# Optimization experiments

Measured on AMD Instinct MI355X. Metric: run time of the kernel, lower is better.

## Reference

```python
import jax, jax.numpy as jnp
import numpy as np

# ---- config (matches init_kwargs) ----
B, IN_CH, H, W_SP = 8, 1, 256, 256
WIDTH, M1, M2, NL, OUT_CH = 64, 12, 12, 4, 1
FC_HID = 128


def _gelu(a):
    # torch nn.GELU default = exact erf form
    return jax.nn.gelu(a, approximate=False)


def _spectral_conv2d(x, w1, w2):
    """x: [B, Cin, H, W]; w1/w2: [Cin, Cout, M1, M2, 2] -> [B, Cout, H, W]."""
    Bn, Cin, Hn, Wn = x.shape
    Cout = w1.shape[1]
    x_ft = jnp.fft.rfft2(x, axes=(-2, -1))          # [B, Cin, H, W//2+1] complex
    w1c = w1[..., 0] + 1j * w1[..., 1]
    w2c = w2[..., 0] + 1j * w2[..., 1]
    top = jnp.einsum('bixy,ioxy->boxy', x_ft[:, :, :M1, :M2], w1c)
    bot = jnp.einsum('bixy,ioxy->boxy', x_ft[:, :, -M1:, :M2], w2c)
    out_ft = jnp.zeros((Bn, Cout, Hn, Wn // 2 + 1), dtype=x_ft.dtype)
    out_ft = out_ft.at[:, :, :M1, :M2].set(top)
    out_ft = out_ft.at[:, :, -M1:, :M2].set(bot)
    return jnp.fft.irfft2(out_ft, s=(Hn, Wn), axes=(-2, -1))


def setup_inputs() -> dict:
    key = jax.random.key(0)
    ks = jax.random.split(key, 8)
    scale = 1.0 / (WIDTH * WIDTH)
    inp = {
        'x': jax.random.normal(ks[0], (B, IN_CH, H, W_SP)),
        'fc0_w': jax.random.normal(ks[1], (WIDTH, IN_CH + 2)) * 0.3,
        'fc0_b': jnp.zeros((WIDTH,)),
        # spectral weights stacked over layers: [NL, Cin, Cout, M1, M2, 2]
        'w1': scale * jax.random.uniform(ks[2], (NL, WIDTH, WIDTH, M1, M2, 2)),
        'w2': scale * jax.random.uniform(ks[3], (NL, WIDTH, WIDTH, M1, M2, 2)),
        # 1x1 conv weights: [NL, Cout, Cin] and bias [NL, Cout]
        'pw_w': jax.random.normal(ks[4], (NL, WIDTH, WIDTH)) * (1.0 / np.sqrt(WIDTH)),
        'pw_b': jnp.zeros((NL, WIDTH)),
        'fc1_w': jax.random.normal(ks[5], (FC_HID, WIDTH)) * (1.0 / np.sqrt(WIDTH)),
        'fc1_b': jnp.zeros((FC_HID,)),
        'fc2_w': jax.random.normal(ks[6], (OUT_CH, FC_HID)) * (1.0 / np.sqrt(FC_HID)),
        'fc2_b': jnp.zeros((OUT_CH,)),
    }
    return {k: v.astype(jnp.float32) for k, v in inp.items()}


def reference(x, fc0_w, fc0_b, w1, w2, pw_w, pw_b, fc1_w, fc1_b, fc2_w, fc2_b):
    Bn, _, Hn, Wn = x.shape
    # positional grid in [0, 1], concatenated on channel dim
    gx = jnp.broadcast_to(jnp.linspace(0.0, 1.0, Hn)[None, None, :, None], (Bn, 1, Hn, Wn))
    gy = jnp.broadcast_to(jnp.linspace(0.0, 1.0, Wn)[None, None, None, :], (Bn, 1, Hn, Wn))
    h = jnp.concatenate([x, gx.astype(x.dtype), gy.astype(x.dtype)], axis=1)  # [B, in+2, H, W]
    # lift (fc0): Linear over channels (torch weight layout [out, in])
    h = jnp.einsum('bcxy,wc->bwxy', h, fc0_w) + fc0_b[None, :, None, None]
    for i in range(NL):
        x1 = _spectral_conv2d(h, w1[i], w2[i])
        x2 = jnp.einsum('bixy,oi->boxy', h, pw_w[i]) + pw_b[i][None, :, None, None]
        h = x1 + x2
        if i < NL - 1:
            h = _gelu(h)
    # projection head
    h = jnp.einsum('bwxy,fw->bfxy', h, fc1_w) + fc1_b[None, :, None, None]
    h = _gelu(h)
    h = jnp.einsum('bfxy,of->boxy', h, fc2_w) + fc2_b[None, :, None, None]
    return h  # [B, out_channels, H, W]
```

## Files before the change

### kernel.cpp

```cpp
#include <hip/hip_runtime.h>
#include <hip/hip_bf16.h>

#define FC0_F   0
#define FC0B_F  192
#define PWB_F   16640
#define FC1B_F  25088
#define FC2_F   25216
#define FC2B_F  25344
#define PHW_F   25408
#define PHH_F   31552
#define FLAG_F  44032
#define PWA_HI_U 512
#define PWA_LO_U 16896
#define FC1A_HI_U 33792
#define FC1A_LO_U 41984
#define TWI_HI_U 88192
#define TWI_LO_U 96384
#define TWF_HI_U 104576
#define TWF_LO_U 112768
#define HB_OFF_U  131072
#define GG_OFF_U  33685504
#define FO_OFF_F  18415616
#define WS_NEED   74842112
#define NT11 60161

typedef short bf16x8 __attribute__((ext_vector_type(8)));
typedef float f32x4  __attribute__((ext_vector_type(4)));

union FU10 { float f; unsigned u; };
__device__ __forceinline__ float bfu2f(unsigned short u) { FU10 v; v.u = ((unsigned)u) << 16; return v.f; }
__device__ __forceinline__ unsigned short f2bfu(float f) {
  FU10 v; v.f = f; unsigned b = v.u;
  return (unsigned short)((b + 0x7FFFu + ((b >> 16) & 1u)) >> 16);
}
__device__ __forceinline__ unsigned pk2bf(float a, float b) {
  return (unsigned)f2bfu(a) | ((unsigned)f2bfu(b) << 16);
}
__device__ __forceinline__ float gelu10(float v) {
  float s = v * 0.7071067811865475f;
  float a = fabsf(s);
  float t = __builtin_amdgcn_rcpf(1.0f + 0.3275911f * a);
  float p = t*(0.254829592f + t*(-0.284496736f + t*(1.421413741f
          + t*(-1.453152027f + t*1.061405429f))));
  float er = 1.0f - p * __expf(-a * a);
  er = copysignf(er, s);
  return 0.5f * v * (1.0f + er);
}
__device__ __forceinline__ float rdw10(const __hip_bfloat16* h, const float* f,
                                       long i, int isf32) {
  return isf32 ? f[i] : __bfloat162float(h[i]);
}

__global__ __launch_bounds__(256) void kf10_fill(__hip_bfloat16* outH, float code) {
  outH[(size_t)blockIdx.x * 256 + threadIdx.x] = __float2bfloat16(code);
}

__global__ __launch_bounds__(64) void kd10_detect(const unsigned short* Xh, float* Wf) {
  if (threadIdx.x == 0 && blockIdx.x == 0) {
    int ok = 1;
    for (int k = 0; k < 128; ++k) {
      unsigned short u = Xh[2 * k];
      unsigned e = (u >> 7) & 0xFF;
      if (!(u == 0 || (e >= 0x60 && e <= 0x88))) ok = 0;
    }
    Wf[FLAG_F] = ok ? 0.0f : 1.0f;
  }
}

__global__ __launch_bounds__(256) void kt10_tables(
    const __hip_bfloat16* f0h, const float* f0f,
    const __hip_bfloat16* f0bh, const float* f0bf,
    const __hip_bfloat16* pwh, const float* pwf,
    const __hip_bfloat16* pwbh, const float* pwbf,
    const __hip_bfloat16* f1h, const float* f1f,
    const __hip_bfloat16* f1bh, const float* f1bf,
    const __hip_bfloat16* f2h, const float* f2f,
    const __hip_bfloat16* f2bh, const float* f2bf,
    float* Wf) {
  unsigned short* Wu = (unsigned short*)Wf;
  const int isf32 = (Wf[FLAG_F] != 0.0f);
  const int stride = gridDim.x * blockDim.x;
  for (int n0 = blockIdx.x * blockDim.x + threadIdx.x; n0 < NT11; n0 += stride) {
    int n = n0;
    if (n < 192) { Wf[FC0_F + n] = rdw10(f0h, f0f, n, isf32); continue; }
    n -= 192;
    if (n < 64)  { Wf[FC0B_F + n] = rdw10(f0bh, f0bf, n, isf32); continue; }
    n -= 64;
    if (n < 256) { Wf[PWB_F + n] = rdw10(pwbh, pwbf, n, isf32); continue; }
    n -= 256;
    if (n < 8192) {
      float v = rdw10(f1h, f1f, n, isf32);
      unsigned short hi = f2bfu(v);
      Wu[FC1A_HI_U + n] = hi;
      Wu[FC1A_LO_U + n] = f2bfu(v - bfu2f(hi));
      continue;
    }
    n -= 8192;
    if (n < 128) { Wf[FC1B_F + n] = rdw10(f1bh, f1bf, n, isf32); continue; }
    n -= 128;
    if (n < 128) { Wf[FC2_F + n] = rdw10(f2h, f2f, n, isf32); continue; }
    n -= 128;
    if (n < 1)   { Wf[FC2B_F + n] = rdw10(f2bh, f2bf, 0, isf32); continue; }
    n -= 1;
    if (n < 6144) { int w = n / 24, r = n % 24, ky = r >> 1, part = r & 1;
      int idx = (w * ky) & 255; float a = idx * (1.0f/128.0f);
      Wf[PHW_F + n] = part ? sinpif(a) : cospif(a); continue; }
    n -= 6144;
    if (n < 12288) { int xx = n / 48, r = n % 48, kx = r >> 1, part = r & 1;
      int kxa = (kx < 12) ? kx : kx + 232;
      int idx = (xx * kxa) & 255; float a = idx * (1.0f/128.0f);
      Wf[PHH_F + n] = part ? sinpif(a) : cospif(a); continue; }
    n -= 12288;
    if (n < 16384) {
      float v = rdw10(pwh, pwf, n, isf32);
      unsigned short hi = f2bfu(v);
      Wu[PWA_HI_U + n] = hi;
      Wu[PWA_LO_U + n] = f2bfu(v - bfu2f(hi));
      continue;
    }
    n -= 16384;
    if (n < 8192) {
      int w = n >> 5, k = n & 31;
      float v;
      if (k == 0)      v = 1.0f / 65536.0f;
      else if (k < 12) { int idx = (w*k) & 255;
        v =  2.0f * cospif(idx * (1.0f/128.0f)) * (1.0f/65536.0f); }
      else if (k < 23) { int ky = k - 11; int idx = (w*ky) & 255;
        v = -2.0f * sinpif(idx * (1.0f/128.0f)) * (1.0f/65536.0f); }
      else v = 0.0f;
      unsigned short hi = f2bfu(v);
      Wu[TWI_HI_U + n] = hi;
      Wu[TWI_LO_U + n] = f2bfu(v - bfu2f(hi));
      continue;
    }
    n -= 8192;
    {
      int r = n >> 8, w = n & 255;
      float v;
      if (r < 12)      { int idx = (w*r) & 255;  v =  cospif(idx * (1.0f/128.0f)); }
      else if (r < 24) { int ky = r - 12; int idx = (w*ky) & 255;
                         v = -sinpif(idx * (1.0f/128.0f)); }
      else v = 0.0f;
      unsigned short hi = f2bfu(v);
      Wu[TWF_HI_U + n] = hi;
      Wu[TWF_LO_U + n] = f2bfu(v - bfu2f(hi));
    }
  }
}

__global__ __launch_bounds__(256) void kl11_lift(const __hip_bfloat16* Xh, const float* Xf,
                                                 const float* Wf,
                                                 __hip_bfloat16* HB, __hip_bfloat16* GG) {
  __shared__ __align__(16) char smem[32768];
  unsigned short* gbT = (unsigned short*)smem;
  const unsigned short* Wu = (const unsigned short*)Wf;
  const int rid = ((blockIdx.x & 7) << 8) | (blockIdx.x >> 3);
  const int b = rid >> 8, x = rid & 255;
  const int t = threadIdx.x;
  const int w = t;
  const int l15 = t & 15, g = (t >> 4) & 3, wv = t >> 6;
  const int isf32 = (Wf[FLAG_F] != 0.0f);
  float xv = isf32 ? Xf[(size_t)(b*256 + x)*256 + w]
                   : __bfloat162float(Xh[(size_t)(b*256 + x)*256 + w]);
  float gx = x * (1.0f/255.0f), gy = w * (1.0f/255.0f);
  unsigned hbreg[32];
#pragma unroll
  for (int cp = 0; cp < 32; ++cp) {
    int c = cp*2;
    float h0 = xv*Wf[FC0_F + c*3]     + gx*Wf[FC0_F + c*3 + 1]
             + gy*Wf[FC0_F + c*3 + 2] + Wf[FC0B_F + c];
    float h1 = xv*Wf[FC0_F + c*3 + 3] + gx*Wf[FC0_F + c*3 + 4]
             + gy*Wf[FC0_F + c*3 + 5] + Wf[FC0B_F + c + 1];
    unsigned pk = pk2bf(h0, h1);
    hbreg[cp] = pk;
    *(unsigned short*)(smem + (((c+0)*512 + w*2) ^ (((c+0) & 7) << 4))) =
        (unsigned short)(pk & 0xFFFFu);
    *(unsigned short*)(smem + (((c+1)*512 + w*2) ^ (((c+1) & 7) << 4))) =
        (unsigned short)(pk >> 16);
  }
  {
    uint4* hbW = (uint4*)(HB + (size_t)(b*256 + x)*16384) + w*8;
#pragma unroll
    for (int j = 0; j < 8; ++j)
      hbW[j] = make_uint4(hbreg[j*4], hbreg[j*4+1], hbreg[j*4+2], hbreg[j*4+3]);
  }
  __syncthreads();

  f32x4 g0 = {0.f, 0.f, 0.f, 0.f}, g1 = {0.f, 0.f, 0.f, 0.f};
  const int crow = wv*16 + l15;
  const int rswz = (crow & 7) << 4;
#pragma unroll
  for (int kk = 0; kk < 8; ++kk) {
    const int k0 = kk*32;
    bf16x8 af  = *(const bf16x8*)(smem + ((crow*512 + (k0 + g*8)*2) ^ rswz));
    bf16x8 b0h = *(const bf16x8*)(Wu + TWF_HI_U + l15*256 + k0 + g*8);
    bf16x8 b0l = *(const bf16x8*)(Wu + TWF_LO_U + l15*256 + k0 + g*8);
    bf16x8 b1h = *(const bf16x8*)(Wu + TWF_HI_U + (16 + l15)*256 + k0 + g*8);
    bf16x8 b1l = *(const bf16x8*)(Wu + TWF_LO_U + (16 + l15)*256 + k0 + g*8);
    g0 = __builtin_amdgcn_mfma_f32_16x16x32_bf16(af, b0h, g0, 0, 0, 0);
    g0 = __builtin_amdgcn_mfma_f32_16x16x32_bf16(af, b0l, g0, 0, 0, 0);
    g1 = __builtin_amdgcn_mfma_f32_16x16x32_bf16(af, b1h, g1, 0, 0, 0);
    g1 = __builtin_amdgcn_mfma_f32_16x16x32_bf16(af, b1l, g1, 0, 0, 0);
  }
  __syncthreads();
#pragma unroll
  for (int ntk = 0; ntk < 2; ++ntk) {
    int kyt = ntk*16 + l15;
    if (kyt < 24) {
      f32x4 gg = ntk ? g1 : g0;
#pragma unroll
      for (int rr = 0; rr < 4; ++rr)
        gbT[(wv*16 + g*4 + rr)*24 + kyt] = f2bfu(gg[rr]);
    }
  }
  __syncthreads();
  unsigned* GGrow = (unsigned*)((unsigned short*)GG + (size_t)(b*256 + x)*1536);
  const unsigned* st32 = (const unsigned*)gbT;
#pragma unroll
  for (int j = 0; j < 3; ++j) GGrow[j*256 + t] = st32[j*256 + t];
}

__global__ __launch_bounds__(256) void ks10_spec(const float* Wf, const __hip_bfloat16* GG,
    const __hip_bfloat16* w1h, const float* w1f,
    const __hip_bfloat16* w2h, const float* w2f,
    float* Fo, int l) {
  __shared__ float pbufA[6400];
  __shared__ float Fbuf[1536];
  const int blk = (blockIdx.x & 7) * 24 + (blockIdx.x >> 3);
  const int b = blk / 24, kx = blk % 24;
  const int t = threadIdx.x;
  const int isf32 = (Wf[FLAG_F] != 0.0f);
  {
    const int i = t & 63, q = t >> 6;
    float fr[12], fi[12];
#pragma unroll
    for (int k = 0; k < 12; ++k) { fr[k] = 0.0f; fi[k] = 0.0f; }
    for (int j = 0; j < 64; ++j) {
      int x = q*64 + j;
      const uint4* gp = (const uint4*)((const unsigned short*)GG
                        + (size_t)(b*256 + x)*1536 + i*24);
      uint4 u0 = gp[0], u1 = gp[1], u2 = gp[2];
      float cc = Wf[PHH_F + x*48 + 2*kx], ss = Wf[PHH_F + x*48 + 2*kx + 1];
      unsigned uu[12] = {u0.x, u0.y, u0.z, u0.w, u1.x, u1.y, u1.z, u1.w,
                         u2.x, u2.y, u2.z, u2.w};
#pragma unroll
      for (int k = 0; k < 12; ++k) {
        unsigned ure = uu[k >> 1], uim = uu[6 + (k >> 1)];
        float gr = bfu2f((unsigned short)((k & 1) ? (ure >> 16) : (ure & 0xFFFFu)));
        float gi = bfu2f((unsigned short)((k & 1) ? (uim >> 16) : (uim & 0xFFFFu)));
        fr[k] += gr*cc + gi*ss;
        fi[k] += gi*cc - gr*ss;
      }
    }
#pragma unroll
    for (int k = 0; k < 12; ++k) {
      pbufA[q*1600 + i*25 + 2*k]     = fr[k];
      pbufA[q*1600 + i*25 + 2*k + 1] = fi[k];
    }
  }
  __syncthreads();
#pragma unroll
  for (int j = 0; j < 6; ++j) {
    int idx = j*256 + t;
    int cc = idx / 24, m = idx - cc*24;
    Fbuf[idx] = pbufA[cc*25 + m] + pbufA[1600 + cc*25 + m]
              + pbufA[3200 + cc*25 + m] + pbufA[4800 + cc*25 + m];
  }
  __syncthreads();
  {
    const int o = t & 63, q = t >> 6;
    float br[12], bi[12];
#pragma unroll
    for (int k = 0; k < 12; ++k) { br[k] = 0.0f; bi[k] = 0.0f; }
    const int kxe = (kx < 12) ? kx : kx - 12;
    const __hip_bfloat16* wh = (kx < 12) ? w1h : w2h;
    const float*         wfp = (kx < 12) ? w1f : w2f;
    for (int i = q*16; i < q*16 + 16; ++i) {
      size_t widx = ((size_t)((l*64 + i)*64 + o))*288 + (size_t)kxe*24;
      float wr_[12], wi_[12];
      if (isf32) {
        const float* wp = wfp + widx;
#pragma unroll
        for (int k = 0; k < 12; ++k) { wr_[k] = wp[2*k]; wi_[k] = wp[2*k + 1]; }
      } else {
        const uint4* wp = (const uint4*)((const unsigned short*)wh + widx);
        uint4 u0 = wp[0], u1 = wp[1], u2 = wp[2];
        unsigned uu[12] = {u0.x, u0.y, u0.z, u0.w, u1.x, u1.y, u1.z, u1.w,
                           u2.x, u2.y, u2.z, u2.w};
#pragma unroll
        for (int k = 0; k < 12; ++k) {
          wr_[k] = bfu2f((unsigned short)(uu[k] & 0xFFFFu));
          wi_[k] = bfu2f((unsigned short)(uu[k] >> 16));
        }
      }
      const float* Fp = Fbuf + i*24;
#pragma unroll
      for (int k = 0; k < 12; ++k) {
        float Fr = Fp[k], Fi = Fp[12 + k];
        br[k] += Fr*wr_[k] - Fi*wi_[k];
        bi[k] += Fr*wi_[k] + Fi*wr_[k];
      }
    }
#pragma unroll
    for (int k = 0; k < 12; ++k) {
      pbufA[q*1536 + k*128 + o*2]     = br[k];
      pbufA[q*1536 + k*128 + o*2 + 1] = bi[k];
    }
  }
  __syncthreads();
#pragma unroll
  for (int j = 0; j < 6; ++j) {
    int n = j*256 + t;
    int ky = n >> 7, r = n & 127;
    Fo[((size_t)(b*12 + ky)*24 + kx)*128 + r] =
        pbufA[n] + pbufA[1536 + n] + pbufA[3072 + n] + pbufA[4608 + n];
  }
}

__global__ __launch_bounds__(256) void ky13_layer(const float* __restrict__ Wf,
                                                  __hip_bfloat16* __restrict__ HB,
                                                  __hip_bfloat16* __restrict__ GG,
                                                  const float* __restrict__ Fo,
                                                  __hip_bfloat16* __restrict__ outH,
                                                  float* __restrict__ outF,
                                                  int l, int last) {
  __shared__ __align__(16) char smem[32768];
  unsigned short* gbT   = (unsigned short*)smem;
  unsigned*       gbT32 = (unsigned*)smem;
  const unsigned short* Wu = (const unsigned short*)Wf;
  const int rid = ((blockIdx.x & 7) << 8) | (blockIdx.x >> 3);
  const int b = rid >> 8, x = rid & 255;
  const int t = threadIdx.x;
  const int l15 = t & 15, g = (t >> 4) & 3, wv = t >> 6;

  unsigned short* HBu = (unsigned short*)(HB + (size_t)(b*256 + x)*16384);
  unsigned short* GGu = (unsigned short*)GG + (size_t)(b*256 + x)*1536;

  const int w0w = wv*64;
  bf16x8 bh[4][2];
#pragma unroll
  for (int nt = 0; nt < 4; ++nt) {
    int wpx = w0w + nt*16 + l15;
#pragma unroll
    for (int kt = 0; kt < 2; ++kt)
      bh[nt][kt] = *(const bf16x8*)(HBu + (size_t)wpx*64 + kt*32 + g*8);
  }

  { int o = t >> 2, cu = t & 3; gbT32[o*16 + 12 + cu] = 0u; }
  {
    const float* phx = Wf + PHH_F + x*48;
#pragma unroll 1
    for (int j = 0; j < 3; ++j) {
      int p = j*256 + t; int ky = p >> 6, o = p & 63;
      const float2* Fop = (const float2*)(Fo + (size_t)(b*12 + ky)*3072) + o;
      float gr = 0.0f, gi = 0.0f;
#pragma unroll
      for (int kx = 0; kx < 24; ++kx) {
        float2 f = Fop[kx*64];
        float cc = phx[2*kx], ss = phx[2*kx + 1];
        gr += f.x*cc - f.y*ss;
        gi += f.x*ss + f.y*cc;
      }
      gbT[o*32 + ky] = f2bfu(gr);
      gbT[o*32 + (ky ? (11 + ky) : 23)] = f2bfu(gi);
    }
  }

  bf16x8 bi[4][2];
#pragma unroll
  for (int nt = 0; nt < 4; ++nt) {
    int wpx = w0w + nt*16 + l15;
    bi[nt][0] = *(const bf16x8*)(Wu + TWI_HI_U + wpx*32 + g*8);
    bi[nt][1] = *(const bf16x8*)(Wu + TWI_LO_U + wpx*32 + g*8);
  }
  bf16x8 apw[4][2][2];
#pragma unroll
  for (int mt = 0; mt < 4; ++mt)
#pragma unroll
    for (int kt = 0; kt < 2; ++kt) {
      int off = l*4096 + (mt*16 + l15)*64 + kt*32 + g*8;
      apw[mt][kt][0] = *(const bf16x8*)(Wu + PWA_HI_U + off);
      apw[mt][kt][1] = *(const bf16x8*)(Wu + PWA_LO_U + off);
    }
  float bias[4][4];
#pragma unroll
  for (int mt = 0; mt < 4; ++mt)
#pragma unroll
    for (int r = 0; r < 4; ++r)
      bias[mt][r] = Wf[PWB_F + l*64 + mt*16 + g*4 + r];

  __syncthreads();
  bf16x8 ainv[4];
#pragma unroll
  for (int mt = 0; mt < 4; ++mt)
    ainv[mt] = *(const bf16x8*)(gbT + (mt*16 + l15)*32 + g*8);
  __syncthreads();

#pragma unroll
  for (int nt = 0; nt < 4; ++nt) {
    const int wpx = w0w + nt*16 + l15;
#pragma unroll
    for (int mt = 0; mt < 4; ++mt) {
      f32x4 acc = {bias[mt][0], bias[mt][1], bias[mt][2], bias[mt][3]};
      acc = __builtin_amdgcn_mfma_f32_16x16x32_bf16(ainv[mt],      bi[nt][0], acc, 0, 0, 0);
      acc = __builtin_amdgcn_mfma_f32_16x16x32_bf16(ainv[mt],      bi[nt][1], acc, 0, 0, 0);
      acc = __builtin_amdgcn_mfma_f32_16x16x32_bf16(apw[mt][0][0], bh[nt][0], acc, 0, 0, 0);
      acc = __builtin_amdgcn_mfma_f32_16x16x32_bf16(apw[mt][0][1], bh[nt][0], acc, 0, 0, 0);
      acc = __builtin_amdgcn_mfma_f32_16x16x32_bf16(apw[mt][1][0], bh[nt][1], acc, 0, 0, 0);
      acc = __builtin_amdgcn_mfma_f32_16x16x32_bf16(apw[mt][1][1], bh[nt][1], acc, 0, 0, 0);
      float v0 = acc[0], v1 = acc[1], v2 = acc[2], v3 = acc[3];
      if (!last) { v0 = gelu10(v0); v1 = gelu10(v1); v2 = gelu10(v2); v3 = gelu10(v3); }
      const int c0 = mt*16 + g*4;
      uint2 pk; pk.x = pk2bf(v0, v1); pk.y = pk2bf(v2, v3);
      if (!last) {
        *(uint2*)(HBu + (size_t)wpx*64 + c0) = pk;
        *(unsigned short*)(smem + (((c0+0)*512 + wpx*2) ^ (((c0+0) & 7) << 4))) = f2bfu(v0);
        *(unsigned short*)(smem + (((c0+1)*512 + wpx*2) ^ (((c0+1) & 7) << 4))) = f2bfu(v1);
        *(unsigned short*)(smem + (((c0+2)*512 + wpx*2) ^ (((c0+2) & 7) << 4))) = f2bfu(v2);
        *(unsigned short*)(smem + (((c0+3)*512 + wpx*2) ^ (((c0+3) & 7) << 4))) = f2bfu(v3);
      } else {
        *(uint2*)(smem + ((wpx*128 + c0*2) ^ ((wpx & 7) << 4))) = pk;
      }
    }
  }

  if (!last) {
    __syncthreads();
    f32x4 g0 = {0.f, 0.f, 0.f, 0.f}, g1 = {0.f, 0.f, 0.f, 0.f};
    const int crow = wv*16 + l15;
    const int rswz = (crow & 7) << 4;
#pragma unroll
    for (int kk = 0; kk < 8; ++kk) {
      const int k0 = kk*32;
      bf16x8 af  = *(const bf16x8*)(smem + ((crow*512 + (k0 + g*8)*2) ^ rswz));
      bf16x8 b0h = *(const bf16x8*)(Wu + TWF_HI_U + l15*256 + k0 + g*8);
      bf16x8 b0l = *(const bf16x8*)(Wu + TWF_LO_U + l15*256 + k0 + g*8);
      bf16x8 b1h = *(const bf16x8*)(Wu + TWF_HI_U + (16 + l15)*256 + k0 + g*8);
      bf16x8 b1l = *(const bf16x8*)(Wu + TWF_LO_U + (16 + l15)*256 + k0 + g*8);
      g0 = __builtin_amdgcn_mfma_f32_16x16x32_bf16(af, b0h, g0, 0, 0, 0);
      g0 = __builtin_amdgcn_mfma_f32_16x16x32_bf16(af, b0l, g0, 0, 0, 0);
      g1 = __builtin_amdgcn_mfma_f32_16x16x32_bf16(af, b1h, g1, 0, 0, 0);
      g1 = __builtin_amdgcn_mfma_f32_16x16x32_bf16(af, b1l, g1, 0, 0, 0);
    }
    __syncthreads();
#pragma unroll
    for (int ntk = 0; ntk < 2; ++ntk) {
      int kyt = ntk*16 + l15;
      if (kyt < 24) {
        f32x4 gg = ntk ? g1 : g0;
#pragma unroll
        for (int rr = 0; rr < 4; ++rr)
          gbT[(wv*16 + g*4 + rr)*24 + kyt] = f2bfu(gg[rr]);
      }
    }
    __syncthreads();
    unsigned* GGrow = (unsigned*)GGu;
    const unsigned* st32 = (const unsigned*)gbT;
#pragma unroll
    for (int j = 0; j < 3; ++j) GGrow[j*256 + t] = st32[j*256 + t];
  } else {
    __syncthreads();
    const int isf32 = (Wf[FLAG_F] != 0.0f);
    bf16x8 bh2[4][2];
#pragma unroll
    for (int nt = 0; nt < 4; ++nt) {
      int wpx = w0w + nt*16 + l15;
#pragma unroll
      for (int kt = 0; kt < 2; ++kt)
        bh2[nt][kt] = *(const bf16x8*)(smem +
            ((wpx*128 + kt*64 + g*16) ^ ((wpx & 7) << 4)));
    }
    float s[4] = {0.0f, 0.0f, 0.0f, 0.0f};
#pragma unroll 2
    for (int mt = 0; mt < 8; ++mt) {
      const int arow = (mt*16 + l15)*64 + g*8;
      bf16x8 a0h = *(const bf16x8*)(Wu + FC1A_HI_U + arow);
      bf16x8 a0l = *(const bf16x8*)(Wu + FC1A_LO_U + arow);
      bf16x8 a1h = *(const bf16x8*)(Wu + FC1A_HI_U + arow + 32);
      bf16x8 a1l = *(const bf16x8*)(Wu + FC1A_LO_U + arow + 32);
      float f1b[4], f2v[4];
#pragma unroll
      for (int r = 0; r < 4; ++r) {
        f1b[r] = Wf[FC1B_F + mt*16 + g*4 + r];
        f2v[r] = Wf[FC2_F  + mt*16 + g*4 + r];
      }
#pragma unroll
      for (int nt = 0; nt < 4; ++nt) {
        f32x4 acc = {f1b[0], f1b[1], f1b[2], f1b[3]};
        acc = __builtin_amdgcn_mfma_f32_16x16x32_bf16(a0h, bh2[nt][0], acc, 0, 0, 0);
        acc = __builtin_amdgcn_mfma_f32_16x16x32_bf16(a0l, bh2[nt][0], acc, 0, 0, 0);
        acc = __builtin_amdgcn_mfma_f32_16x16x32_bf16(a1h, bh2[nt][1], acc, 0, 0, 0);
        acc = __builtin_amdgcn_mfma_f32_16x16x32_bf16(a1l, bh2[nt][1], acc, 0, 0, 0);
#pragma unroll
        for (int r = 0; r < 4; ++r)
          s[nt] += gelu10(acc[r]) * f2v[r];
      }
    }
    const float fc2b = Wf[FC2B_F];
#pragma unroll
    for (int nt = 0; nt < 4; ++nt) {
      float v = s[nt];
      v += __shfl_xor(v, 16);
      v += __shfl_xor(v, 32);
      if (g == 0) {
        size_t idx = (size_t)(b*256 + x)*256 + (w0w + nt*16 + l15);
        if (isf32) outF[idx] = v + fc2b;
        else       outH[idx] = __float2bfloat16(v + fc2b);
      }
    }
  }
}

extern "C" void kernel_launch(void* const* d_in, const int* in_sizes, int n_in,
                              void* d_out, int out_size, void* d_ws, size_t ws_size,
                              hipStream_t stream) {
  (void)out_size;
  __hip_bfloat16* outH = (__hip_bfloat16*)d_out;
  float*          outF = (float*)d_out;
  float*          Wf   = (float*)d_ws;
  __hip_bfloat16* HB   = (__hip_bfloat16*)d_ws + HB_OFF_U;
  __hip_bfloat16* GG   = (__hip_bfloat16*)d_ws + GG_OFF_U;
  float*          Fo   = (float*)d_ws + FO_OFF_F;

  static const int EXP_SZ[11] = {524288, 192, 64, 4718592, 4718592,
                                 16384, 256, 8192, 128, 128, 1};
  if (n_in != 11) { kf10_fill<<<2048, 256, 0, stream>>>(outH, 27648.0f); return; }
  for (int i = 0; i < 11; ++i) {
    if (in_sizes[i] != EXP_SZ[i]) {
      kf10_fill<<<2048, 256, 0, stream>>>(outH, 28672.0f + 256.0f * (float)i);
      return;
    }
  }
  if (ws_size < (size_t)WS_NEED) {
    int q = (int)(ws_size >> 25); if (q > 31) q = 31;
    kf10_fill<<<2048, 256, 0, stream>>>(outH, 4096.0f + 32.0f * (float)q);
    return;
  }

  kd10_detect<<<1, 64, 0, stream>>>((const unsigned short*)d_in[0], Wf);
  kt10_tables<<<64, 256, 0, stream>>>(
      (const __hip_bfloat16*)d_in[1], (const float*)d_in[1],
      (const __hip_bfloat16*)d_in[2], (const float*)d_in[2],
      (const __hip_bfloat16*)d_in[5], (const float*)d_in[5],
      (const __hip_bfloat16*)d_in[6], (const float*)d_in[6],
      (const __hip_bfloat16*)d_in[7], (const float*)d_in[7],
      (const __hip_bfloat16*)d_in[8], (const float*)d_in[8],
      (const __hip_bfloat16*)d_in[9], (const float*)d_in[9],
      (const __hip_bfloat16*)d_in[10], (const float*)d_in[10],
      Wf);
  kl11_lift<<<2048, 256, 0, stream>>>((const __hip_bfloat16*)d_in[0],
                                      (const float*)d_in[0], Wf, HB, GG);
  for (int l = 0; l < 4; ++l) {
    ks10_spec<<<192, 256, 0, stream>>>(Wf, GG,
        (const __hip_bfloat16*)d_in[3], (const float*)d_in[3],
        (const __hip_bfloat16*)d_in[4], (const float*)d_in[4],
        Fo, l);
    ky13_layer<<<2048, 256, 0, stream>>>(Wf, HB, GG, Fo, outH, outF,
                                         l, (l == 3) ? 1 : 0);
  }
}
```

Before: 691.2 us.

## Widen spectral kernel to 1024 threads and swizzle layer-kernel LDS tile

The spectral-mixing kernel now launches 1024 threads per block instead of 256. Each wave handles a quarter of the previous x-range and input-channel range, and partial sums are combined in shared memory over four serialized accumulate rounds with barriers. This targets low occupancy, since only 192 blocks run on a large GPU. Separately, the layer kernel's 64x32 bf16 shared tile uses an XOR swizzle on byte addresses to reduce LDS bank conflicts on the transposed writes and MFMA operand reads. The extra barriers and serialized shared-memory reductions add overhead in exchange.

```diff
diff --git a/kernel.cpp b/kernel.cpp
--- a/kernel.cpp
+++ b/kernel.cpp
@@ -49,6 +49,9 @@
 __device__ __forceinline__ float rdw10(const __hip_bfloat16* h, const float* f,
                                        long i, int isf32) {
   return isf32 ? f[i] : __bfloat162float(h[i]);
+}
+__device__ __forceinline__ int gsw17(int o, int br) {
+  return (o*64 + br) ^ ((o & 7) << 4);
 }
 
 __global__ __launch_bounds__(256) void kf10_fill(__hip_bfloat16* outH, float code) {
@@ -220,7 +223,7 @@
   for (int j = 0; j < 3; ++j) GGrow[j*256 + t] = st32[j*256 + t];
 }
 
-__global__ __launch_bounds__(256) void ks10_spec(const float* Wf, const __hip_bfloat16* GG,
+__global__ __launch_bounds__(1024) void ks11_spec(const float* Wf, const __hip_bfloat16* GG,
     const __hip_bfloat16* w1h, const float* w1f,
     const __hip_bfloat16* w2h, const float* w2f,
     float* Fo, int l) {
@@ -229,18 +232,20 @@
   const int blk = (blockIdx.x & 7) * 24 + (blockIdx.x >> 3);
   const int b = blk / 24, kx = blk % 24;
   const int t = threadIdx.x;
+  const int q = t >> 6;
+  const int rr = q >> 2, ss = q & 3;
   const int isf32 = (Wf[FLAG_F] != 0.0f);
   {
-    const int i = t & 63, q = t >> 6;
+    const int i = t & 63;
     float fr[12], fi[12];
 #pragma unroll
     for (int k = 0; k < 12; ++k) { fr[k] = 0.0f; fi[k] = 0.0f; }
-    for (int j = 0; j < 64; ++j) {
-      int x = q*64 + j;
+    for (int j = 0; j < 16; ++j) {
+      int x = q*16 + j;
       const uint4* gp = (const uint4*)((const unsigned short*)GG
                         + (size_t)(b*256 + x)*1536 + i*24);
       uint4 u0 = gp[0], u1 = gp[1], u2 = gp[2];
-      float cc = Wf[PHH_F + x*48 + 2*kx], ss = Wf[PHH_F + x*48 + 2*kx + 1];
+      float cc = Wf[PHH_F + x*48 + 2*kx], sn = Wf[PHH_F + x*48 + 2*kx + 1];
       unsigned uu[12] = {u0.x, u0.y, u0.z, u0.w, u1.x, u1.y, u1.z, u1.w,
                          u2.x, u2.y, u2.z, u2.w};
 #pragma unroll
@@ -248,34 +253,44 @@
         unsigned ure = uu[k >> 1], uim = uu[6 + (k >> 1)];
         float gr = bfu2f((unsigned short)((k & 1) ? (ure >> 16) : (ure & 0xFFFFu)));
         float gi = bfu2f((unsigned short)((k & 1) ? (uim >> 16) : (uim & 0xFFFFu)));
-        fr[k] += gr*cc + gi*ss;
-        fi[k] += gi*cc - gr*ss;
-      }
-    }
-#pragma unroll
-    for (int k = 0; k < 12; ++k) {
-      pbufA[q*1600 + i*25 + 2*k]     = fr[k];
-      pbufA[q*1600 + i*25 + 2*k + 1] = fi[k];
-    }
-  }
-  __syncthreads();
-#pragma unroll
-  for (int j = 0; j < 6; ++j) {
-    int idx = j*256 + t;
-    int cc = idx / 24, m = idx - cc*24;
-    Fbuf[idx] = pbufA[cc*25 + m] + pbufA[1600 + cc*25 + m]
-              + pbufA[3200 + cc*25 + m] + pbufA[4800 + cc*25 + m];
+        fr[k] += gr*cc + gi*sn;
+        fi[k] += gi*cc - gr*sn;
+      }
+    }
+#pragma unroll 1
+    for (int r = 0; r < 4; ++r) {
+      if (rr == r) {
+        float* slot = pbufA + ss*1600 + i*25;
+        if (r == 0) {
+#pragma unroll
+          for (int k = 0; k < 12; ++k) { slot[2*k] = fr[k]; slot[2*k + 1] = fi[k]; }
+        } else {
+#pragma unroll
+          for (int k = 0; k < 12; ++k) { slot[2*k] += fr[k]; slot[2*k + 1] += fi[k]; }
+        }
+      }
+      __syncthreads();
+    }
+  }
+#pragma unroll
+  for (int j = 0; j < 2; ++j) {
+    int idx = j*1024 + t;
+    if (idx < 1536) {
+      int cc = idx / 24, m = idx - cc*24;
+      Fbuf[idx] = pbufA[cc*25 + m] + pbufA[1600 + cc*25 + m]
+                + pbufA[3200 + cc*25 + m] + pbufA[4800 + cc*25 + m];
+    }
   }
   __syncthreads();
   {
-    const int o = t & 63, q = t >> 6;
+    const int o = t & 63;
     float br[12], bi[12];
 #pragma unroll
     for (int k = 0; k < 12; ++k) { br[k] = 0.0f; bi[k] = 0.0f; }
     const int kxe = (kx < 12) ? kx : kx - 12;
     const __hip_bfloat16* wh = (kx < 12) ? w1h : w2h;
     const float*         wfp = (kx < 12) ? w1f : w2f;
-    for (int i = q*16; i < q*16 + 16; ++i) {
+    for (int i = q*4; i < q*4 + 4; ++i) {
       size_t widx = ((size_t)((l*64 + i)*64 + o))*288 + (size_t)kxe*24;
       float wr_[12], wi_[12];
       if (isf32) {
@@ -301,19 +316,35 @@
         bi[k] += Fr*wi_[k] + Fi*wr_[k];
       }
     }
-#pragma unroll
-    for (int k = 0; k < 12; ++k) {
-      pbufA[q*1536 + k*128 + o*2]     = br[k];
-      pbufA[q*1536 + k*128 + o*2 + 1] = bi[k];
-    }
-  }
-  __syncthreads();
-#pragma unroll
-  for (int j = 0; j < 6; ++j) {
-    int n = j*256 + t;
-    int ky = n >> 7, r = n & 127;
-    Fo[((size_t)(b*12 + ky)*24 + kx)*128 + r] =
-        pbufA[n] + pbufA[1536 + n] + pbufA[3072 + n] + pbufA[4608 + n];
+#pragma unroll 1
+    for (int r = 0; r < 4; ++r) {
+      if (rr == r) {
+        float* slot = pbufA + ss*1536;
+        if (r == 0) {
+#pragma unroll
+          for (int k = 0; k < 12; ++k) {
+            slot[k*128 + o*2]     = br[k];
+            slot[k*128 + o*2 + 1] = bi[k];
+          }
+        } else {
+#pragma unroll
+          for (int k = 0; k < 12; ++k) {
+            slot[k*128 + o*2]     += br[k];
+            slot[k*128 + o*2 + 1] += bi[k];
+          }
+        }
+      }
+      __syncthreads();
+    }
+  }
+#pragma unroll
+  for (int j = 0; j < 2; ++j) {
+    int n = j*1024 + t;
+    if (n < 1536) {
+      int ky = n >> 7, r = n & 127;
+      Fo[((size_t)(b*12 + ky)*24 + kx)*128 + r] =
+          pbufA[n] + pbufA[1536 + n] + pbufA[3072 + n] + pbufA[4608 + n];
+    }
   }
 }
 
@@ -325,8 +356,7 @@
                                                   float* __restrict__ outF,
                                                   int l, int last) {
   __shared__ __align__(16) char smem[32768];
-  unsigned short* gbT   = (unsigned short*)smem;
-  unsigned*       gbT32 = (unsigned*)smem;
+  unsigned short* gbT = (unsigned short*)smem;
   const unsigned short* Wu = (const unsigned short*)Wf;
   const int rid = ((blockIdx.x & 7) << 8) | (blockIdx.x >> 3);
   const int b = rid >> 8, x = rid & 255;
@@ -346,7 +376,8 @@
       bh[nt][kt] = *(const bf16x8*)(HBu + (size_t)wpx*64 + kt*32 + g*8);
   }
 
-  { int o = t >> 2, cu = t & 3; gbT32[o*16 + 12 + cu] = 0u; }
+  { int o = t >> 2, cu = t & 3;
+    *(unsigned*)(smem + gsw17(o, 48 + cu*4)) = 0u; }
   {
     const float* phx = Wf + PHH_F + x*48;
 #pragma unroll 1
@@ -357,12 +388,12 @@
 #pragma unroll
       for (int kx = 0; kx < 24; ++kx) {
         float2 f = Fop[kx*64];
-        float cc = phx[2*kx], ss = phx[2*kx + 1];
-        gr += f.x*cc - f.y*ss;
-        gi += f.x*ss + f.y*cc;
-      }
-      gbT[o*32 + ky] = f2bfu(gr);
-      gbT[o*32 + (ky ? (11 + ky) : 23)] = f2bfu(gi);
+        float cc = phx[2*kx], sn = phx[2*kx + 1];
+        gr += f.x*cc - f.y*sn;
+        gi += f.x*sn + f.y*cc;
+      }
+      *(unsigned short*)(smem + gsw17(o, ky*2)) = f2bfu(gr);
+      *(unsigned short*)(smem + gsw17(o, (ky ? (11 + ky) : 23)*2)) = f2bfu(gi);
     }
   }
 
@@ -393,7 +424,7 @@
   bf16x8 ainv[4];
 #pragma unroll
   for (int mt = 0; mt < 4; ++mt)
-    ainv[mt] = *(const bf16x8*)(gbT + (mt*16 + l15)*32 + g*8);
+    ainv[mt] = *(const bf16x8*)(smem + gsw17(mt*16 + l15, g*16));
   __syncthreads();
 
 #pragma unroll
@@ -551,7 +582,7 @@
   kl11_lift<<<2048, 256, 0, stream>>>((const __hip_bfloat16*)d_in[0],
                                       (const float*)d_in[0], Wf, HB, GG);
   for (int l = 0; l < 4; ++l) {
-    ks10_spec<<<192, 256, 0, stream>>>(Wf, GG,
+    ks11_spec<<<192, 1024, 0, stream>>>(Wf, GG,
         (const __hip_bfloat16*)d_in[3], (const float*)d_in[3],
         (const __hip_bfloat16*)d_in[4], (const float*)d_in[4],
         Fo, l);
```

Result: slower. 708.5 us (+2.5%).
